# Performance work log

Hardware: AMD Instinct MI355X
Metric: run time of the kernel (lower is better)

The kernel has to match this reference:

```python
import jax, jax.numpy as jnp
import numpy as np

VOICED_RATIO = 0.7  # paper: 7:3 voiced/unvoiced output budget
B, C, F_IN, T_IN = 64, 1, 128, 4096
F_OUT, T_OUT = 128, 6144


def setup_inputs() -> dict:
    key = jax.random.key(0)
    k1, k2 = jax.random.split(key)
    mel = jax.random.normal(k1, (B, C, F_IN, T_IN), dtype=jnp.float32)
    vu_mask = jax.random.randint(k2, (B, T_IN), 0, 2, dtype=jnp.int32)
    return {"mel": mel, "vu_mask": vu_mask, "F_out": F_OUT, "T_out": T_OUT}


def _time_maps(mask, T_out):
    """Per-batch composed time mapping.

    Reproduces: (1) run-length V/UV segmentation, (2) per-segment target lengths
    round(rv*L) / round(ruv*L) with the last segment taking the remainder,
    (3) per-segment bilinear (align_corners=False) resample, concatenated,
    (4) final bilinear resize of the concatenated length T_total -> T_out.
    Steps (3) and (4) are composed analytically into gather indices/weights
    directly into the input time axis, so no data-dependent shapes appear.
    Returns indices/weights (each (T_out,)): a0,a1,wa for floor concat index,
    b0,b1,wb for ceil concat index, and lam the second-pass blend weight.
    """
    T_in = mask.shape[0]
    ratio = VOICED_RATIO / (1.0 - VOICED_RATIO)
    # run-length segments: seg_id[t] = index of segment containing frame t
    change = jnp.concatenate([jnp.ones((1,), jnp.int32), (mask[1:] != mask[:-1]).astype(jnp.int32)])
    seg_id = jnp.cumsum(change) - 1
    n_segs = seg_id[-1] + 1
    seg_len = jax.ops.segment_sum(jnp.ones((T_in,), jnp.float32), seg_id, num_segments=T_in)
    seg_voiced = jax.ops.segment_sum(mask.astype(jnp.float32), seg_id, num_segments=T_in) > 0
    len_v = jnp.sum(mask).astype(jnp.float32)
    len_uv = T_in - len_v
    both = (len_v > 0) & (len_uv > 0)
    rv = jnp.where(both, T_out / (len_v + len_uv / ratio),
         jnp.where(len_v > 0, T_out / jnp.maximum(len_v, 1.0), T_out / jnp.maximum(len_uv, 1.0)))
    ruv = jnp.where(both, rv / ratio, rv)
    seg_scale = jnp.where(seg_voiced, rv, ruv)
    idx = jnp.arange(T_in)
    valid = idx < n_segs
    last = idx == (n_segs - 1)
    tgt = jnp.maximum(1.0, jnp.round(seg_scale * seg_len)).astype(jnp.int32)
    tgt = jnp.where(valid & ~last, tgt, 0)
    tgt = jnp.where(last, jnp.maximum(1, T_out - jnp.sum(tgt)), tgt)  # last seg takes remainder
    cum_end = jnp.cumsum(tgt)              # output-space segment ends (concatenated)
    cum_start = cum_end - tgt
    T_total = cum_end[-1]                  # concatenated length (usually == T_out)
    seg_start = jnp.cumsum(seg_len) - seg_len  # input-space segment starts

    def concat_to_input(k):
        # map concatenated output index k -> bilinear gather into input time axis
        s = jnp.minimum(jnp.searchsorted(cum_end, k, side='right'), T_in - 1)
        L = seg_len[s]
        TL = jnp.maximum(tgt[s].astype(jnp.float32), 1.0)
        kl = (k - cum_start[s]).astype(jnp.float32)
        src = jnp.maximum((kl + 0.5) * (L / TL) - 0.5, 0.0)  # align_corners=False
        x0 = jnp.floor(src)
        w = src - x0
        x1 = jnp.minimum(x0 + 1.0, L - 1.0)  # clamp within the segment
        base = seg_start[s]
        return (base + x0).astype(jnp.int32), (base + x1).astype(jnp.int32), w

    # second-pass (final resize) time coordinates; identity when T_total == T_out
    t = jnp.arange(T_out, dtype=jnp.float32)
    sc = jnp.maximum((t + 0.5) * (T_total.astype(jnp.float32) / T_out) - 0.5, 0.0)
    k0 = jnp.floor(sc).astype(jnp.int32)
    k1 = jnp.minimum(k0 + 1, T_total - 1)
    lam = sc - k0.astype(jnp.float32)
    a0, a1, wa = concat_to_input(k0)
    b0, b1, wb = concat_to_input(k1)
    return a0, a1, wa, b0, b1, wb, lam


def _forward(mel, vu_mask, F_out, T_out):
    Bc, Cc, Fc, Tc = mel.shape
    a0, a1, wa, b0, b1, wb, lam = jax.vmap(lambda m: _time_maps(m, T_out))(vu_mask)

    def gt(ix):  # gather along input time axis: (B,T_out) -> (B,C,F,T_out)
        return jnp.take_along_axis(mel, ix[:, None, None, :], axis=3)

    def ex(w):
        return w[:, None, None, :]

    v = ex(1.0 - lam) * (ex(1.0 - wa) * gt(a0) + ex(wa) * gt(a1)) \
      + ex(lam) * (ex(1.0 - wb) * gt(b0) + ex(wb) * gt(b1))  # (B,C,F,T_out)

    # frequency resample F -> F_out (identity when equal), align_corners=False
    f = jnp.arange(F_out, dtype=jnp.float32)
    fs = jnp.maximum((f + 0.5) * (Fc / F_out) - 0.5, 0.0)
    fy0 = jnp.floor(fs).astype(jnp.int32)
    fy1 = jnp.minimum(fy0 + 1, Fc - 1)
    fw = (fs - fy0.astype(jnp.float32))[None, None, :, None]
    return (1.0 - fw) * v[:, :, fy0, :] + fw * v[:, :, fy1, :]


def reference(mel, vu_mask, F_out, T_out):
    return _forward(mel, vu_mask, F_out, T_out)
```

## Files before the change

kernel.cpp:

```cpp
#include <hip/hip_runtime.h>

#define TIN   4096
#define FIN   128
#define NB    64
#define FOUT  128
#define TOUT  6144
#define SEG_STRIDE (3 * TIN + 64)

#define TB    512
#define SPAN  416
#define SPANP (SPAN + 4)
#define SPAN4 (SPAN / 4)
#define FG    8
#define ZSPL  4
#define FPB   (FOUT / ZSPL)
#define NCH   (FPB / FG)

typedef float f32x4 __attribute__((ext_vector_type(4)));
typedef float f32x2 __attribute__((ext_vector_type(2)));

__device__ __forceinline__ int wave_iscan(int v, int lane) {
#pragma unroll
    for (int d = 1; d < 64; d <<= 1) {
        int n = __shfl_up(v, d, 64);
        if (lane >= d) v += n;
    }
    return v;
}

__device__ __forceinline__ int block_scan_incl(int v, int tid, int* wsum4, int* total) {
    const int lane = tid & 63, wid = tid >> 6;
    int incl = wave_iscan(v, lane);
    if (lane == 63) wsum4[wid] = incl;
    __syncthreads();
    int woff = 0;
#pragma unroll
    for (int i = 0; i < 3; ++i) woff += (i < wid) ? wsum4[i] : 0;
    *total = wsum4[0] + wsum4[1] + wsum4[2] + wsum4[3];
    __syncthreads();
    return incl + woff;
}

__global__ __launch_bounds__(256) void seg_kernel(const int* __restrict__ mask,
                                                  int* __restrict__ ws) {
    __shared__ int seg_start_sh[TIN];
    __shared__ int tgt_sh[TIN];
    __shared__ int wsum4[4];

    const int b = blockIdx.x;
    const int tid = threadIdx.x;
    const int* mrow = mask + (size_t)b * TIN;

    for (int i = tid; i < TIN; i += 256) tgt_sh[i] = 0;

    const int base = tid * 16;
    int m[16];
#pragma unroll
    for (int j = 0; j < 4; ++j) {
        int4 v = ((const int4*)(mrow + base))[j];
        m[4 * j + 0] = v.x; m[4 * j + 1] = v.y; m[4 * j + 2] = v.z; m[4 * j + 3] = v.w;
    }
    const int prev = (base == 0) ? 0 : mrow[base - 1];

    int incl[16];
    int run = 0, vsum = 0;
#pragma unroll
    for (int j = 0; j < 16; ++j) {
        int pm = (j == 0) ? prev : m[j - 1];
        int c = (base + j == 0) ? 1 : ((m[j] != pm) ? 1 : 0);
        run += c;
        incl[j] = run;
        vsum += m[j];
    }
    int tot_packed;
    int sp = block_scan_incl((run << 16) | vsum, tid, wsum4, &tot_packed);
    const int n_segs  = tot_packed >> 16;
    const int total_v = tot_packed & 0xFFFF;
    int off = (sp >> 16) - run;
#pragma unroll
    for (int j = 0; j < 16; ++j) {
        int c = (j == 0) ? incl[0] : (incl[j] - incl[j - 1]);
        if (c) seg_start_sh[off + incl[j] - 1] = (base + j) | (m[j] << 16);
    }
    __syncthreads();

    const float len_v = (float)total_v;
    const float len_uv = (float)TIN - len_v;
    const float ratiof = (float)(0.7 / 0.3);
    const bool both = (len_v > 0.f) && (len_uv > 0.f);
    float rv;
    if (both)              rv = (float)TOUT / (len_v + len_uv / ratiof);
    else if (len_v > 0.f)  rv = (float)TOUT / fmaxf(len_v, 1.f);
    else                   rv = (float)TOUT / fmaxf(len_uv, 1.f);
    const float ruv = both ? (rv / ratiof) : rv;

    int lsum = 0;
    for (int s = tid; s < n_segs; s += 256) {
        int v = seg_start_sh[s];
        int st = v & 0xFFFF;
        int voiced = v >> 16;
        int en = (s + 1 < n_segs) ? (seg_start_sh[s + 1] & 0xFFFF) : TIN;
        int len = en - st;
        float scale = voiced ? rv : ruv;
        int tg = (int)fmaxf(1.0f, rintf(scale * (float)len));
        if (s != n_segs - 1) { tgt_sh[s] = tg; lsum += tg; }
    }
    int sum_others;
    block_scan_incl(lsum, tid, wsum4, &sum_others);
    if (tid == 0) tgt_sh[n_segs - 1] = max(1, TOUT - sum_others);
    __syncthreads();

    int tincl[16];
    int trun = 0;
#pragma unroll
    for (int j = 0; j < 16; ++j) { trun += tgt_sh[base + j]; tincl[j] = trun; }
    int ttot;
    int tsincl = block_scan_incl(trun, tid, wsum4, &ttot);
    int toff = tsincl - trun;

    int* wbp = ws + (size_t)b * SEG_STRIDE;
#pragma unroll
    for (int j = 0; j < 16; ++j) {
        int i = base + j;
        if (i < n_segs) wbp[2 * TIN + i] = toff + tincl[j];
    }
    for (int i = tid; i < n_segs; i += 256) {
        wbp[i]       = seg_start_sh[i] & 0xFFFF;
        wbp[TIN + i] = tgt_sh[i];
    }
    if (tid == 0) { wbp[3 * TIN] = n_segs; wbp[3 * TIN + 1] = ttot; }
}

__device__ __forceinline__ void map_concat(int k, const unsigned short* __restrict__ cum16,
                                           const int* __restrict__ wbp, int n_segs,
                                           int& i0, int& i1, float& w) {
    int lo = 0, hi = n_segs;
    while (lo < hi) {
        int mid = (lo + hi) >> 1;
        if ((int)cum16[mid] > k) hi = mid; else lo = mid + 1;
    }
    int s = min(lo, n_segs - 1);

    int ce = (int)cum16[s];
    int tg = wbp[TIN + s];
    int cs = ce - tg;
    int st = wbp[s];
    int en = (s + 1 < n_segs) ? wbp[s + 1] : TIN;
    float L  = (float)(en - st);
    float TL = fmaxf((float)tg, 1.f);
    float src = fmaxf(((float)(k - cs) + 0.5f) * (L / TL) - 0.5f, 0.f);
    float x0 = floorf(src);
    w = src - x0;
    float x1 = fminf(x0 + 1.f, L - 1.f);
    i0 = st + (int)x0;
    i1 = st + (int)x1;
}

__global__ __launch_bounds__(256) void resample_kernel(const float* __restrict__ mel,
                                                       const int* __restrict__ ws,
                                                       float* __restrict__ out) {
    __shared__ unsigned short cum16[TIN];
    __shared__ float stage[2][FG * SPANP];
    __shared__ int bcast[2];

    const int b = blockIdx.y;
    const int tid = threadIdx.x;
    const int t0 = blockIdx.x * TB + tid * 2;
    const int fz = blockIdx.z * FPB;

    const int* wbp = ws + (size_t)b * SEG_STRIDE;
    const int n_segs  = wbp[3 * TIN];
    const int T_total = wbp[3 * TIN + 1];

    for (int i = tid; i < n_segs; i += 256) cum16[i] = (unsigned short)wbp[2 * TIN + i];
    __syncthreads();

    const bool identity = (T_total == TOUT);

    int A0[2], A1[2], B0[2], B1[2];
    float W0[2], W1[2], W2[2], W3[2];
#pragma unroll
    for (int j = 0; j < 2; ++j) {
        const int t = t0 + j;
        int k0, k1; float lam;
        if (identity) {
            k0 = t; k1 = t; lam = 0.f;
        } else {
            float sc = fmaxf(((float)t + 0.5f) * ((float)T_total / (float)TOUT) - 0.5f, 0.f);
            k0 = (int)floorf(sc);
            k1 = min(k0 + 1, T_total - 1);
            lam = sc - (float)k0;
        }
        int a0, a1, bb0, bb1; float wa, wb;
        map_concat(k0, cum16, wbp, n_segs, a0, a1, wa);
        if (identity) { bb0 = a0; bb1 = a1; wb = wa; }
        else          map_concat(k1, cum16, wbp, n_segs, bb0, bb1, wb);
        A0[j] = a0; A1[j] = a1; B0[j] = bb0; B1[j] = bb1;
        W0[j] = (1.f - lam) * (1.f - wa);
        W1[j] = (1.f - lam) * wa;
        W2[j] = lam * (1.f - wb);
        W3[j] = lam * wb;
    }

    if (tid == 0)   bcast[0] = A0[0];
    if (tid == 255) bcast[1] = max(A1[1], B1[1]);
    __syncthreads();
    const int x_lo = bcast[0] & ~3;
    const int x_hi = bcast[1];
    const int n4 = (x_hi + 1 - x_lo + 3) >> 2;

    if (n4 <= SPAN4) {
        const int row = tid >> 5;
        const int c0  = tid & 31;
        const int a0r0 = A0[0] - x_lo, b0r0 = B0[0] - x_lo;
        const int a0r1 = A0[1] - x_lo, b0r1 = B0[1] - x_lo;
        const bool sa0 = (A1[0] == A0[0] + 1), sb0 = (B1[0] == B0[0] + 1);
        const bool sa1 = (A1[1] == A0[1] + 1), sb1 = (B1[1] == B0[1] + 1);

        f32x4 R[4];
#define STAGE_LOAD(ch)                                                                    \
        { const f32x4* gs = (const f32x4*)(mel + ((size_t)(b * FIN + fz + (ch) * FG + row)) * TIN + x_lo); \
          _Pragma("unroll")                                                               \
          for (int k = 0; k < 4; ++k) { int c = c0 + 32 * k; if (c < n4) R[k] = gs[c]; } }
#define STAGE_WRITE(buf)                                                                  \
        { f32x4* ds = (f32x4*)(stage[buf] + row * SPANP);                                 \
          _Pragma("unroll")                                                               \
          for (int k = 0; k < 4; ++k) { int c = c0 + 32 * k; if (c < n4) ds[c] = R[k]; } }

        STAGE_LOAD(0)
        STAGE_WRITE(0)
        __syncthreads();

        for (int ch = 0; ch < NCH; ++ch) {
            const int cur = ch & 1;
            if (ch + 1 < NCH) STAGE_LOAD(ch + 1)

            float* ob = out + ((size_t)(b * FOUT + fz + ch * FG)) * TOUT + t0;
            if (identity) {
#pragma unroll
                for (int f = 0; f < FG; ++f) {
                    const float* Lp = stage[cur] + f * SPANP;
                    float xa0 = Lp[a0r0], ya0 = Lp[a0r0 + 1];
                    float xa1 = Lp[a0r1], ya1 = Lp[a0r1 + 1];
                    f32x2 v;
                    v.x = W0[0] * xa0 + W1[0] * (sa0 ? ya0 : xa0);
                    v.y = W0[1] * xa1 + W1[1] * (sa1 ? ya1 : xa1);
                    __builtin_nontemporal_store(v, (f32x2*)(ob + (size_t)f * TOUT));
                }
            } else {
#pragma unroll
                for (int f = 0; f < FG; ++f) {
                    const float* Lp = stage[cur] + f * SPANP;
                    float xa0 = Lp[a0r0], ya0 = Lp[a0r0 + 1];
                    float xa1 = Lp[a0r1], ya1 = Lp[a0r1 + 1];
                    float xb0 = Lp[b0r0], yb0 = Lp[b0r0 + 1];
                    float xb1 = Lp[b0r1], yb1 = Lp[b0r1 + 1];
                    f32x2 v;
                    v.x = W0[0] * xa0 + W1[0] * (sa0 ? ya0 : xa0) + W2[0] * xb0 + W3[0] * (sb0 ? yb0 : xb0);
                    v.y = W0[1] * xa1 + W1[1] * (sa1 ? ya1 : xa1) + W2[1] * xb1 + W3[1] * (sb1 ? yb1 : xb1);
                    __builtin_nontemporal_store(v, (f32x2*)(ob + (size_t)f * TOUT));
                }
            }

            if (ch + 1 < NCH) STAGE_WRITE(cur ^ 1)
            __syncthreads();
        }
#undef STAGE_LOAD
#undef STAGE_WRITE
    } else {
        const float* mb = mel + (size_t)b * FIN * TIN;
        float* ob = out + ((size_t)(b * FOUT + fz)) * TOUT + t0;
#pragma unroll 4
        for (int f = 0; f < FPB; ++f) {
            const float* r = mb + (size_t)(fz + f) * TIN;
            ob[(size_t)f * TOUT + 0] = W0[0] * r[A0[0]] + W1[0] * r[A1[0]] + W2[0] * r[B0[0]] + W3[0] * r[B1[0]];
            ob[(size_t)f * TOUT + 1] = W0[1] * r[A0[1]] + W1[1] * r[A1[1]] + W2[1] * r[B0[1]] + W3[1] * r[B1[1]];
        }
    }
}

extern "C" void kernel_launch(void* const* d_in, const int* in_sizes, int n_in,
                              void* d_out, int out_size, void* d_ws, size_t ws_size,
                              hipStream_t stream) {
    const float* mel = (const float*)d_in[0];
    const int* mask  = (const int*)d_in[1];
    float* out = (float*)d_out;
    int* ws = (int*)d_ws;

    seg_kernel<<<NB, 256, 0, stream>>>(mask, ws);

    dim3 grid(TOUT / TB, NB, ZSPL);
    resample_kernel<<<grid, 256, 0, stream>>>(mel, ws, out);
}
```

Measured before the change: 79.98 us.

## Precompute per-time gather maps in separate kernel and stage all rows at once

```diff
diff --git a/kernel.cpp b/kernel.cpp
--- a/kernel.cpp
+++ b/kernel.cpp
@@ -7,14 +7,17 @@
 #define TOUT  6144
 #define SEG_STRIDE (3 * TIN + 64)
 
+#define MAPP_OFF (SEG_STRIDE * NB)
+#define MAPW_OFF (MAPP_OFF + NB * TOUT)
+#define WS_NEED  ((size_t)(MAPW_OFF + NB * TOUT * 4) * 4)
+
 #define TB    512
 #define SPAN  416
 #define SPANP (SPAN + 4)
 #define SPAN4 (SPAN / 4)
-#define FG    8
-#define ZSPL  4
+#define ZSPL  8
 #define FPB   (FOUT / ZSPL)
-#define NCH   (FPB / FG)
+#define NLD   7
 
 typedef float f32x4 __attribute__((ext_vector_type(4)));
 typedef float f32x2 __attribute__((ext_vector_type(2)));
@@ -131,16 +134,167 @@
     if (tid == 0) { wbp[3 * TIN] = n_segs; wbp[3 * TIN + 1] = ttot; }
 }
 
-__device__ __forceinline__ void map_concat(int k, const unsigned short* __restrict__ cum16,
-                                           const int* __restrict__ wbp, int n_segs,
-                                           int& i0, int& i1, float& w) {
+__device__ __forceinline__ void map_concat_g(int k, const int* __restrict__ wbp, int n_segs,
+                                             int& i0, int& i1, float& w) {
+    const int* cum = wbp + 2 * TIN;
+    int lo = 0, hi = n_segs;
+    while (lo < hi) {
+        int mid = (lo + hi) >> 1;
+        if (cum[mid] > k) hi = mid; else lo = mid + 1;
+    }
+    int s = min(lo, n_segs - 1);
+
+    int ce = cum[s];
+    int tg = wbp[TIN + s];
+    int cs = ce - tg;
+    int st = wbp[s];
+    int en = (s + 1 < n_segs) ? wbp[s + 1] : TIN;
+    float L  = (float)(en - st);
+    float TL = fmaxf((float)tg, 1.f);
+    float src = fmaxf(((float)(k - cs) + 0.5f) * (L / TL) - 0.5f, 0.f);
+    float x0 = floorf(src);
+    w = src - x0;
+    float x1 = fminf(x0 + 1.f, L - 1.f);
+    i0 = st + (int)x0;
+    i1 = st + (int)x1;
+}
+
+__global__ __launch_bounds__(256) void map_kernel(const int* __restrict__ ws,
+                                                  int* __restrict__ mapP,
+                                                  float* __restrict__ mapW) {
+    const int b = blockIdx.y;
+    const int t = blockIdx.x * 256 + threadIdx.x;
+    const int* wbp = ws + (size_t)b * SEG_STRIDE;
+    const int n_segs  = wbp[3 * TIN];
+    const int T_total = wbp[3 * TIN + 1];
+    const bool identity = (T_total == TOUT);
+
+    int k0, k1; float lam;
+    if (identity) {
+        k0 = t; k1 = t; lam = 0.f;
+    } else {
+        float sc = fmaxf(((float)t + 0.5f) * ((float)T_total / (float)TOUT) - 0.5f, 0.f);
+        k0 = (int)floorf(sc);
+        k1 = min(k0 + 1, T_total - 1);
+        lam = sc - (float)k0;
+    }
+    int a0, a1, bb0, bb1; float wa, wb;
+    map_concat_g(k0, wbp, n_segs, a0, a1, wa);
+    if (identity) { bb0 = a0; bb1 = a1; wb = wa; }
+    else          map_concat_g(k1, wbp, n_segs, bb0, bb1, wb);
+
+    unsigned p = (unsigned)a0 | ((a1 != a0) ? (1u << 13) : 0u) | (identity ? (1u << 14) : 0u)
+               | ((unsigned)bb0 << 16) | ((bb1 != bb0) ? (1u << 29) : 0u);
+    mapP[(size_t)b * TOUT + t] = (int)p;
+    f32x4 w = {(1.f - lam) * (1.f - wa), (1.f - lam) * wa, lam * (1.f - wb), lam * wb};
+    ((f32x4*)mapW)[(size_t)b * TOUT + t] = w;
+}
+
+__global__ __launch_bounds__(256) void resample_kernel(const float* __restrict__ mel,
+                                                       const int* __restrict__ mapP,
+                                                       const float* __restrict__ mapW,
+                                                       float* __restrict__ out) {
+    __shared__ float stage[FPB * SPANP];
+    __shared__ int bcast[2];
+
+    const int b = blockIdx.y;
+    const int tid = threadIdx.x;
+    const int t0 = blockIdx.x * TB + 2 * tid;
+    const int fz = blockIdx.z * FPB;
+
+    const size_t mi = (size_t)b * TOUT + t0;
+    const int2 pp = *(const int2*)(mapP + mi);
+    const f32x4 wv0 = ((const f32x4*)mapW)[mi];
+    const f32x4 wv1 = ((const f32x4*)mapW)[mi + 1];
+    const unsigned p0 = (unsigned)pp.x, p1 = (unsigned)pp.y;
+
+    if (tid == 0) bcast[0] = (int)(p0 & 0x1FFFu);
+    if (tid == 255) {
+        int A1 = (int)(p1 & 0x1FFFu) + (int)((p1 >> 13) & 1u);
+        int B1 = (int)((p1 >> 16) & 0x1FFFu) + (int)((p1 >> 29) & 1u);
+        bcast[1] = max(A1, B1);
+    }
+    __syncthreads();
+    const int x_lo = bcast[0] & ~3;
+    const int x_hi = bcast[1];
+    const int n4 = (x_hi + 1 - x_lo + 3) >> 2;
+    const bool identity = (p0 >> 14) & 1u;
+
+    int a0r0 = (int)(p0 & 0x1FFFu),         a0r1 = (int)(p1 & 0x1FFFu);
+    int b0r0 = (int)((p0 >> 16) & 0x1FFFu), b0r1 = (int)((p1 >> 16) & 0x1FFFu);
+    const bool sa0 = (p0 >> 13) & 1u, sb0 = (p0 >> 29) & 1u;
+    const bool sa1 = (p1 >> 13) & 1u, sb1 = (p1 >> 29) & 1u;
+
+    if (n4 <= SPAN4) {
+        a0r0 -= x_lo; a0r1 -= x_lo; b0r0 -= x_lo; b0r1 -= x_lo;
+        const int row = tid >> 4;
+        const int c0  = tid & 15;
+
+        const f32x4* gs = (const f32x4*)(mel + ((size_t)(b * FIN + fz + row)) * TIN + x_lo);
+        f32x4 R[NLD];
+#pragma unroll
+        for (int k = 0; k < NLD; ++k) { int c = c0 + 16 * k; if (c < n4) R[k] = gs[c]; }
+        f32x4* ds = (f32x4*)(stage + row * SPANP);
+#pragma unroll
+        for (int k = 0; k < NLD; ++k) { int c = c0 + 16 * k; if (c < n4) ds[c] = R[k]; }
+        __syncthreads();
+
+        float* ob = out + ((size_t)(b * FOUT + fz)) * TOUT + t0;
+        if (identity) {
+#pragma unroll
+            for (int f = 0; f < FPB; ++f) {
+                const float* Lp = stage + f * SPANP;
+                float xa0 = Lp[a0r0], ya0 = Lp[a0r0 + 1];
+                float xa1 = Lp[a0r1], ya1 = Lp[a0r1 + 1];
+                f32x2 v;
+                v.x = wv0.x * xa0 + wv0.y * (sa0 ? ya0 : xa0);
+                v.y = wv1.x * xa1 + wv1.y * (sa1 ? ya1 : xa1);
+                __builtin_nontemporal_store(v, (f32x2*)(ob + (size_t)f * TOUT));
+            }
+        } else {
+#pragma unroll
+            for (int f = 0; f < FPB; ++f) {
+                const float* Lp = stage + f * SPANP;
+                float xa0 = Lp[a0r0], ya0 = Lp[a0r0 + 1];
+                float xa1 = Lp[a0r1], ya1 = Lp[a0r1 + 1];
+                float xb0 = Lp[b0r0], yb0 = Lp[b0r0 + 1];
+                float xb1 = Lp[b0r1], yb1 = Lp[b0r1 + 1];
+                f32x2 v;
+                v.x = wv0.x * xa0 + wv0.y * (sa0 ? ya0 : xa0) + wv0.z * xb0 + wv0.w * (sb0 ? yb0 : xb0);
+                v.y = wv1.x * xa1 + wv1.y * (sa1 ? ya1 : xa1) + wv1.z * xb1 + wv1.w * (sb1 ? yb1 : xb1);
+                __builtin_nontemporal_store(v, (f32x2*)(ob + (size_t)f * TOUT));
+            }
+        }
+    } else {
+        const float* mb = mel + (size_t)b * FIN * TIN;
+        float* ob = out + ((size_t)(b * FOUT + fz)) * TOUT + t0;
+#pragma unroll 4
+        for (int f = 0; f < FPB; ++f) {
+            const float* r = mb + (size_t)(fz + f) * TIN;
+            float v0 = wv0.x * r[a0r0] + wv0.y * r[a0r0 + (sa0 ? 1 : 0)]
+                     + wv0.z * r[b0r0] + wv0.w * r[b0r0 + (sb0 ? 1 : 0)];
+            float v1 = wv1.x * r[a0r1] + wv1.y * r[a0r1 + (sa1 ? 1 : 0)]
+                     + wv1.z * r[b0r1] + wv1.w * r[b0r1 + (sb1 ? 1 : 0)];
+            ob[(size_t)f * TOUT + 0] = v0;
+            ob[(size_t)f * TOUT + 1] = v1;
+        }
+    }
+}
+
+#define LFG    8
+#define LZSPL  4
+#define LFPB   (FOUT / LZSPL)
+#define LNCH   (LFPB / LFG)
+
+__device__ __forceinline__ void map_concat_s(int k, const unsigned short* __restrict__ cum16,
+                                             const int* __restrict__ wbp, int n_segs,
+                                             int& i0, int& i1, float& w) {
     int lo = 0, hi = n_segs;
     while (lo < hi) {
         int mid = (lo + hi) >> 1;
         if ((int)cum16[mid] > k) hi = mid; else lo = mid + 1;
     }
     int s = min(lo, n_segs - 1);
-
     int ce = (int)cum16[s];
     int tg = wbp[TIN + s];
     int cs = ce - tg;
@@ -156,17 +310,17 @@
     i1 = st + (int)x1;
 }
 
-__global__ __launch_bounds__(256) void resample_kernel(const float* __restrict__ mel,
+__global__ __launch_bounds__(256) void resample_legacy(const float* __restrict__ mel,
                                                        const int* __restrict__ ws,
                                                        float* __restrict__ out) {
     __shared__ unsigned short cum16[TIN];
-    __shared__ float stage[2][FG * SPANP];
+    __shared__ float stage[2][LFG * SPANP];
     __shared__ int bcast[2];
 
     const int b = blockIdx.y;
     const int tid = threadIdx.x;
     const int t0 = blockIdx.x * TB + tid * 2;
-    const int fz = blockIdx.z * FPB;
+    const int fz = blockIdx.z * LFPB;
 
     const int* wbp = ws + (size_t)b * SEG_STRIDE;
     const int n_segs  = wbp[3 * TIN];
@@ -183,18 +337,17 @@
     for (int j = 0; j < 2; ++j) {
         const int t = t0 + j;
         int k0, k1; float lam;
-        if (identity) {
-            k0 = t; k1 = t; lam = 0.f;
-        } else {
+        if (identity) { k0 = t; k1 = t; lam = 0.f; }
+        else {
             float sc = fmaxf(((float)t + 0.5f) * ((float)T_total / (float)TOUT) - 0.5f, 0.f);
             k0 = (int)floorf(sc);
             k1 = min(k0 + 1, T_total - 1);
             lam = sc - (float)k0;
         }
         int a0, a1, bb0, bb1; float wa, wb;
-        map_concat(k0, cum16, wbp, n_segs, a0, a1, wa);
+        map_concat_s(k0, cum16, wbp, n_segs, a0, a1, wa);
         if (identity) { bb0 = a0; bb1 = a1; wb = wa; }
-        else          map_concat(k1, cum16, wbp, n_segs, bb0, bb1, wb);
+        else          map_concat_s(k1, cum16, wbp, n_segs, bb0, bb1, wb);
         A0[j] = a0; A1[j] = a1; B0[j] = bb0; B1[j] = bb1;
         W0[j] = (1.f - lam) * (1.f - wa);
         W1[j] = (1.f - lam) * wa;
@@ -218,60 +371,47 @@
         const bool sa1 = (A1[1] == A0[1] + 1), sb1 = (B1[1] == B0[1] + 1);
 
         f32x4 R[4];
-#define STAGE_LOAD(ch)                                                                    \
-        { const f32x4* gs = (const f32x4*)(mel + ((size_t)(b * FIN + fz + (ch) * FG + row)) * TIN + x_lo); \
+#define L_STAGE_LOAD(ch)                                                                  \
+        { const f32x4* gs = (const f32x4*)(mel + ((size_t)(b * FIN + fz + (ch) * LFG + row)) * TIN + x_lo); \
           _Pragma("unroll")                                                               \
           for (int k = 0; k < 4; ++k) { int c = c0 + 32 * k; if (c < n4) R[k] = gs[c]; } }
-#define STAGE_WRITE(buf)                                                                  \
+#define L_STAGE_WRITE(buf)                                                                \
         { f32x4* ds = (f32x4*)(stage[buf] + row * SPANP);                                 \
           _Pragma("unroll")                                                               \
           for (int k = 0; k < 4; ++k) { int c = c0 + 32 * k; if (c < n4) ds[c] = R[k]; } }
 
-        STAGE_LOAD(0)
-        STAGE_WRITE(0)
+        L_STAGE_LOAD(0)
+        L_STAGE_WRITE(0)
         __syncthreads();
 
-        for (int ch = 0; ch < NCH; ++ch) {
+        for (int ch = 0; ch < LNCH; ++ch) {
             const int cur = ch & 1;
-            if (ch + 1 < NCH) STAGE_LOAD(ch + 1)
-
-            float* ob = out + ((size_t)(b * FOUT + fz + ch * FG)) * TOUT + t0;
-            if (identity) {
-#pragma unroll
-                for (int f = 0; f < FG; ++f) {
-                    const float* Lp = stage[cur] + f * SPANP;
-                    float xa0 = Lp[a0r0], ya0 = Lp[a0r0 + 1];
-                    float xa1 = Lp[a0r1], ya1 = Lp[a0r1 + 1];
-                    f32x2 v;
-                    v.x = W0[0] * xa0 + W1[0] * (sa0 ? ya0 : xa0);
-                    v.y = W0[1] * xa1 + W1[1] * (sa1 ? ya1 : xa1);
-                    __builtin_nontemporal_store(v, (f32x2*)(ob + (size_t)f * TOUT));
-                }
-            } else {
-#pragma unroll
-                for (int f = 0; f < FG; ++f) {
-                    const float* Lp = stage[cur] + f * SPANP;
-                    float xa0 = Lp[a0r0], ya0 = Lp[a0r0 + 1];
-                    float xa1 = Lp[a0r1], ya1 = Lp[a0r1 + 1];
-                    float xb0 = Lp[b0r0], yb0 = Lp[b0r0 + 1];
-                    float xb1 = Lp[b0r1], yb1 = Lp[b0r1 + 1];
-                    f32x2 v;
-                    v.x = W0[0] * xa0 + W1[0] * (sa0 ? ya0 : xa0) + W2[0] * xb0 + W3[0] * (sb0 ? yb0 : xb0);
-                    v.y = W0[1] * xa1 + W1[1] * (sa1 ? ya1 : xa1) + W2[1] * xb1 + W3[1] * (sb1 ? yb1 : xb1);
-                    __builtin_nontemporal_store(v, (f32x2*)(ob + (size_t)f * TOUT));
-                }
+            if (ch + 1 < LNCH) L_STAGE_LOAD(ch + 1)
+
+            float* ob = out + ((size_t)(b * FOUT + fz + ch * LFG)) * TOUT + t0;
+#pragma unroll
+            for (int f = 0; f < LFG; ++f) {
+                const float* Lp = stage[cur] + f * SPANP;
+                float xa0 = Lp[a0r0], ya0 = Lp[a0r0 + 1];
+                float xa1 = Lp[a0r1], ya1 = Lp[a0r1 + 1];
+                float xb0 = Lp[b0r0], yb0 = Lp[b0r0 + 1];
+                float xb1 = Lp[b0r1], yb1 = Lp[b0r1 + 1];
+                f32x2 v;
+                v.x = W0[0] * xa0 + W1[0] * (sa0 ? ya0 : xa0) + W2[0] * xb0 + W3[0] * (sb0 ? yb0 : xb0);
+                v.y = W0[1] * xa1 + W1[1] * (sa1 ? ya1 : xa1) + W2[1] * xb1 + W3[1] * (sb1 ? yb1 : xb1);
+                __builtin_nontemporal_store(v, (f32x2*)(ob + (size_t)f * TOUT));
             }
 
-            if (ch + 1 < NCH) STAGE_WRITE(cur ^ 1)
+            if (ch + 1 < LNCH) L_STAGE_WRITE(cur ^ 1)
             __syncthreads();
         }
-#undef STAGE_LOAD
-#undef STAGE_WRITE
+#undef L_STAGE_LOAD
+#undef L_STAGE_WRITE
     } else {
         const float* mb = mel + (size_t)b * FIN * TIN;
         float* ob = out + ((size_t)(b * FOUT + fz)) * TOUT + t0;
 #pragma unroll 4
-        for (int f = 0; f < FPB; ++f) {
+        for (int f = 0; f < LFPB; ++f) {
             const float* r = mb + (size_t)(fz + f) * TIN;
             ob[(size_t)f * TOUT + 0] = W0[0] * r[A0[0]] + W1[0] * r[A1[0]] + W2[0] * r[B0[0]] + W3[0] * r[B1[0]];
             ob[(size_t)f * TOUT + 1] = W0[1] * r[A0[1]] + W1[1] * r[A1[1]] + W2[1] * r[B0[1]] + W3[1] * r[B1[1]];
@@ -289,6 +429,15 @@
 
     seg_kernel<<<NB, 256, 0, stream>>>(mask, ws);
 
-    dim3 grid(TOUT / TB, NB, ZSPL);
-    resample_kernel<<<grid, 256, 0, stream>>>(mel, ws, out);
-}
+    if (ws_size >= WS_NEED) {
+        int*   mapP = ws + MAPP_OFF;
+        float* mapW = (float*)(ws + MAPW_OFF);
+        dim3 gmap(TOUT / 256, NB);
+        map_kernel<<<gmap, 256, 0, stream>>>(ws, mapP, mapW);
+        dim3 grid(TOUT / TB, NB, ZSPL);
+        resample_kernel<<<grid, 256, 0, stream>>>(mel, mapP, mapW, out);
+    } else {
+        dim3 grid(TOUT / TB, NB, LZSPL);
+        resample_legacy<<<grid, 256, 0, stream>>>(mel, ws, out);
+    }
+}
```

Measured after the change: 90.61 us. +13.3%, slower.

## Precompute per-window segment offsets and load only a local cumsum window

Applied to the files above, without the earlier changes.

```diff
diff --git a/kernel.cpp b/kernel.cpp
--- a/kernel.cpp
+++ b/kernel.cpp
@@ -8,6 +8,8 @@
 #define SEG_STRIDE (3 * TIN + 64)
 
 #define TB    512
+#define NWIN  (TOUT / TB)
+#define SEGW  768
 #define SPAN  416
 #define SPANP (SPAN + 4)
 #define SPAN4 (SPAN / 4)
@@ -17,7 +19,6 @@
 #define NCH   (FPB / FG)
 
 typedef float f32x4 __attribute__((ext_vector_type(4)));
-typedef float f32x2 __attribute__((ext_vector_type(2)));
 
 __device__ __forceinline__ int wave_iscan(int v, int lane) {
 #pragma unroll
@@ -129,19 +130,36 @@
         wbp[TIN + i] = tgt_sh[i];
     }
     if (tid == 0) { wbp[3 * TIN] = n_segs; wbp[3 * TIN + 1] = ttot; }
-}
-
-__device__ __forceinline__ void map_concat(int k, const unsigned short* __restrict__ cum16,
-                                           const int* __restrict__ wbp, int n_segs,
-                                           int& i0, int& i1, float& w) {
-    int lo = 0, hi = n_segs;
+
+    __syncthreads();
+#pragma unroll
+    for (int j = 0; j < 16; ++j) tgt_sh[base + j] = toff + tincl[j];
+    __syncthreads();
+    if (tid < NWIN) {
+        float sc = fmaxf(((float)(tid * TB) + 0.5f) * ((float)ttot / (float)TOUT) - 0.5f, 0.f);
+        int kf = max((int)floorf(sc) - 2, 0);
+        int lo = 0, hi = n_segs;
+        while (lo < hi) {
+            int mid = (lo + hi) >> 1;
+            if (tgt_sh[mid] > kf) hi = mid; else lo = mid + 1;
+        }
+        wbp[3 * TIN + 2 + tid] = min(lo, n_segs - 1);
+    }
+}
+
+__device__ __forceinline__ void map_concat_w(int k, const unsigned short* __restrict__ cumw,
+                                             int s_lo, const int* __restrict__ wbp, int n_segs,
+                                             int& i0, int& i1, float& w) {
+    int lo = 0, hi = SEGW;
     while (lo < hi) {
         int mid = (lo + hi) >> 1;
-        if ((int)cum16[mid] > k) hi = mid; else lo = mid + 1;
-    }
-    int s = min(lo, n_segs - 1);
-
-    int ce = (int)cum16[s];
+        if ((int)cumw[mid] > k) hi = mid; else lo = mid + 1;
+    }
+    int ce;
+    int s;
+    if (lo < SEGW) { s = min(s_lo + lo, n_segs - 1); ce = (int)cumw[lo]; }
+    else           { s = n_segs - 1; ce = wbp[2 * TIN + s]; }
+
     int tg = wbp[TIN + s];
     int cs = ce - tg;
     int st = wbp[s];
@@ -159,20 +177,24 @@
 __global__ __launch_bounds__(256) void resample_kernel(const float* __restrict__ mel,
                                                        const int* __restrict__ ws,
                                                        float* __restrict__ out) {
-    __shared__ unsigned short cum16[TIN];
+    __shared__ unsigned short cumw[SEGW];
     __shared__ float stage[2][FG * SPANP];
     __shared__ int bcast[2];
 
     const int b = blockIdx.y;
     const int tid = threadIdx.x;
-    const int t0 = blockIdx.x * TB + tid * 2;
+    const int tbase = blockIdx.x * TB;
     const int fz = blockIdx.z * FPB;
 
     const int* wbp = ws + (size_t)b * SEG_STRIDE;
     const int n_segs  = wbp[3 * TIN];
     const int T_total = wbp[3 * TIN + 1];
-
-    for (int i = tid; i < n_segs; i += 256) cum16[i] = (unsigned short)wbp[2 * TIN + i];
+    const int s_lo    = wbp[3 * TIN + 2 + blockIdx.x];
+
+    for (int i = tid; i < SEGW; i += 256) {
+        int s = s_lo + i;
+        cumw[i] = (s < n_segs) ? (unsigned short)wbp[2 * TIN + s] : (unsigned short)0xFFFF;
+    }
     __syncthreads();
 
     const bool identity = (T_total == TOUT);
@@ -181,7 +203,7 @@
     float W0[2], W1[2], W2[2], W3[2];
 #pragma unroll
     for (int j = 0; j < 2; ++j) {
-        const int t = t0 + j;
+        const int t = tbase + tid + j * 256;
         int k0, k1; float lam;
         if (identity) {
             k0 = t; k1 = t; lam = 0.f;
@@ -192,9 +214,9 @@
             lam = sc - (float)k0;
         }
         int a0, a1, bb0, bb1; float wa, wb;
-        map_concat(k0, cum16, wbp, n_segs, a0, a1, wa);
+        map_concat_w(k0, cumw, s_lo, wbp, n_segs, a0, a1, wa);
         if (identity) { bb0 = a0; bb1 = a1; wb = wa; }
-        else          map_concat(k1, cum16, wbp, n_segs, bb0, bb1, wb);
+        else          map_concat_w(k1, cumw, s_lo, wbp, n_segs, bb0, bb1, wb);
         A0[j] = a0; A1[j] = a1; B0[j] = bb0; B1[j] = bb1;
         W0[j] = (1.f - lam) * (1.f - wa);
         W1[j] = (1.f - lam) * wa;
@@ -235,17 +257,17 @@
             const int cur = ch & 1;
             if (ch + 1 < NCH) STAGE_LOAD(ch + 1)
 
-            float* ob = out + ((size_t)(b * FOUT + fz + ch * FG)) * TOUT + t0;
+            float* ob = out + ((size_t)(b * FOUT + fz + ch * FG)) * TOUT + tbase + tid;
             if (identity) {
 #pragma unroll
                 for (int f = 0; f < FG; ++f) {
                     const float* Lp = stage[cur] + f * SPANP;
                     float xa0 = Lp[a0r0], ya0 = Lp[a0r0 + 1];
                     float xa1 = Lp[a0r1], ya1 = Lp[a0r1 + 1];
-                    f32x2 v;
-                    v.x = W0[0] * xa0 + W1[0] * (sa0 ? ya0 : xa0);
-                    v.y = W0[1] * xa1 + W1[1] * (sa1 ? ya1 : xa1);
-                    __builtin_nontemporal_store(v, (f32x2*)(ob + (size_t)f * TOUT));
+                    float vx = W0[0] * xa0 + W1[0] * (sa0 ? ya0 : xa0);
+                    float vy = W0[1] * xa1 + W1[1] * (sa1 ? ya1 : xa1);
+                    __builtin_nontemporal_store(vx, ob + (size_t)f * TOUT);
+                    __builtin_nontemporal_store(vy, ob + (size_t)f * TOUT + 256);
                 }
             } else {
 #pragma unroll
@@ -255,10 +277,10 @@
                     float xa1 = Lp[a0r1], ya1 = Lp[a0r1 + 1];
                     float xb0 = Lp[b0r0], yb0 = Lp[b0r0 + 1];
                     float xb1 = Lp[b0r1], yb1 = Lp[b0r1 + 1];
-                    f32x2 v;
-                    v.x = W0[0] * xa0 + W1[0] * (sa0 ? ya0 : xa0) + W2[0] * xb0 + W3[0] * (sb0 ? yb0 : xb0);
-                    v.y = W0[1] * xa1 + W1[1] * (sa1 ? ya1 : xa1) + W2[1] * xb1 + W3[1] * (sb1 ? yb1 : xb1);
-                    __builtin_nontemporal_store(v, (f32x2*)(ob + (size_t)f * TOUT));
+                    float vx = W0[0] * xa0 + W1[0] * (sa0 ? ya0 : xa0) + W2[0] * xb0 + W3[0] * (sb0 ? yb0 : xb0);
+                    float vy = W0[1] * xa1 + W1[1] * (sa1 ? ya1 : xa1) + W2[1] * xb1 + W3[1] * (sb1 ? yb1 : xb1);
+                    __builtin_nontemporal_store(vx, ob + (size_t)f * TOUT);
+                    __builtin_nontemporal_store(vy, ob + (size_t)f * TOUT + 256);
                 }
             }
 
@@ -269,12 +291,12 @@
 #undef STAGE_WRITE
     } else {
         const float* mb = mel + (size_t)b * FIN * TIN;
-        float* ob = out + ((size_t)(b * FOUT + fz)) * TOUT + t0;
+        float* ob = out + ((size_t)(b * FOUT + fz)) * TOUT + tbase + tid;
 #pragma unroll 4
         for (int f = 0; f < FPB; ++f) {
             const float* r = mb + (size_t)(fz + f) * TIN;
-            ob[(size_t)f * TOUT + 0] = W0[0] * r[A0[0]] + W1[0] * r[A1[0]] + W2[0] * r[B0[0]] + W3[0] * r[B1[0]];
-            ob[(size_t)f * TOUT + 1] = W0[1] * r[A0[1]] + W1[1] * r[A1[1]] + W2[1] * r[B0[1]] + W3[1] * r[B1[1]];
+            ob[(size_t)f * TOUT]       = W0[0] * r[A0[0]] + W1[0] * r[A1[0]] + W2[0] * r[B0[0]] + W3[0] * r[B1[0]];
+            ob[(size_t)f * TOUT + 256] = W0[1] * r[A0[1]] + W1[1] * r[A1[1]] + W2[1] * r[B0[1]] + W3[1] * r[B1[1]];
         }
     }
 }
```

Result: faster. 75.33 us (-5.8%).
